# Kernel tuning notes

Measured on AMD Instinct MI355X. Metric: run time of the kernel, lower is better.

Reference implementation:

```python
import jax, jax.numpy as jnp
import numpy as np

H = 16          # num heads
DH = 64         # head size
D = H * DH      # hidden size 1024
B, S = 2, 2048


def setup_inputs() -> dict:
    key = jax.random.key(0)
    ks = jax.random.split(key, 9)
    scale = 1.0 / np.sqrt(D)
    p = {}
    p["hidden_states"] = jax.random.normal(ks[0], (B, S, D), dtype=jnp.float32)
    for i, name in enumerate(["q", "k", "v", "o"]):
        # stored so that y = x @ W + b (transpose of torch Linear weight)
        p[f"W{name}"] = jax.random.normal(ks[1 + 2 * i], (D, D), dtype=jnp.float32) * scale
        p[f"b{name}"] = jax.random.normal(ks[2 + 2 * i], (D,), dtype=jnp.float32) * 0.01
    return p


def reference(hidden_states, Wq, bq, Wk, bk, Wv, bv, Wo, bo):
    b, s, _ = hidden_states.shape
    q = hidden_states @ Wq + bq  # [B,S,D]
    k = hidden_states @ Wk + bk
    v = hidden_states @ Wv + bv
    # [B,H,S,DH]
    q = q.reshape(b, s, H, DH).transpose(0, 2, 1, 3)
    k = k.reshape(b, s, H, DH).transpose(0, 2, 1, 3)
    v = v.reshape(b, s, H, DH).transpose(0, 2, 1, 3)
    scores = jnp.einsum("bhqd,bhkd->bhqk", q, k) / np.sqrt(DH)
    causal = jnp.triu(jnp.ones((s, s), dtype=bool), k=1)  # True above diagonal -> masked
    scores = jnp.where(causal, -jnp.inf, scores)
    attn = jax.nn.softmax(scores, axis=-1)  # dropout p=0 (eval)
    ctx = jnp.einsum("bhqk,bhkd->bhqd", attn, v)
    ctx = ctx.transpose(0, 2, 1, 3).reshape(b, s, D)
    return ctx @ Wo + bo
```

## Files before the change

### kernel.cpp

```cpp
#include <hip/hip_runtime.h>


typedef _Float16 f16x8 __attribute__((ext_vector_type(8)));
typedef _Float16 f16x4 __attribute__((ext_vector_type(4)));
typedef __fp16 h16x2 __attribute__((ext_vector_type(2)));
typedef float f32x4 __attribute__((ext_vector_type(4)));
typedef float f32x16 __attribute__((ext_vector_type(16)));

#define GLD_LDS16(g, l)                                                        \
  __builtin_amdgcn_global_load_lds(                                            \
      (__attribute__((address_space(1))) const unsigned int*)(g),              \
      (__attribute__((address_space(3))) unsigned int*)(l), 16, 0, 0)

static constexpr int Sdim = 2048;
static constexpr int Ddim = 1024;
static constexpr int NH = 16;
static constexpr int DH = 64;
static constexpr int Mrows = 4096;

static constexpr float QSCALE = 0.125f * 1.44269504f;

struct PrepArgs {
  const float* X;
  _Float16* Y;
  const float *s0, *s1, *s2, *s3;
  _Float16 *d0, *d1, *d2, *d3;
};

__global__ __launch_bounds__(256) void prep(PrepArgs a) {
  __shared__ _Float16 L[64 * 72];
  const int id = blockIdx.x, t = threadIdx.x;
  if (id >= 1024) {
    size_t i = ((size_t)(id - 1024) * 256 + t) * 8;
    float4 f0 = *(const float4*)(a.X + i);
    float4 f1 = *(const float4*)(a.X + i + 4);
    alignas(16) _Float16 h[8] = {(_Float16)f0.x, (_Float16)f0.y, (_Float16)f0.z,
                                 (_Float16)f0.w, (_Float16)f1.x, (_Float16)f1.y,
                                 (_Float16)f1.z, (_Float16)f1.w};
    *(uint4*)(a.Y + i) = *(const uint4*)h;
    return;
  }
  const int z = id >> 8;
  const float* src = z == 0 ? a.s0 : z == 1 ? a.s1 : z == 2 ? a.s2 : a.s3;
  _Float16* dst = z == 0 ? a.d0 : z == 1 ? a.d1 : z == 2 ? a.d2 : a.d3;
  const int k0 = (id & 15) * 64, n0 = ((id >> 4) & 15) * 64;
#pragma unroll
  for (int i = 0; i < 4; ++i) {
    int c = i * 256 + t;
    int row = c >> 4, cc = c & 15;
    float4 f = *(const float4*)&src[(size_t)(k0 + row) * Ddim + n0 + cc * 4];
    L[(cc * 4 + 0) * 72 + row] = (_Float16)f.x;
    L[(cc * 4 + 1) * 72 + row] = (_Float16)f.y;
    L[(cc * 4 + 2) * 72 + row] = (_Float16)f.z;
    L[(cc * 4 + 3) * 72 + row] = (_Float16)f.w;
  }
  __syncthreads();
#pragma unroll
  for (int i = 0; i < 2; ++i) {
    int c = i * 256 + t;
    int n = c >> 3, cc = c & 7;
    *(uint4*)&dst[(size_t)(n0 + n) * Ddim + k0 + cc * 8] =
        *(const uint4*)&L[n * 72 + cc * 8];
  }
}

struct GemmArgs {
  const _Float16* A;
  const _Float16 *Bt0, *Bt1, *Bt2;
  const float *b0, *b1, *b2;
  void *o0, *o1, *o2;
};

template <int MODE, int BN>
__global__ __launch_bounds__(256) void gemmT(GemmArgs g) {
  constexpr int K = 1024;
  constexpr int BK = 64;
  constexpr int WN = BN / 2;
  constexpr int NI = WN / 32;
  constexpr int BCH = BN * 8;
  __shared__ _Float16 As[128 * BK];
  __shared__ _Float16 Bs[BN * BK];
  const int z = blockIdx.z;
  const _Float16* A = g.A;
  const _Float16* Bt = z == 0 ? g.Bt0 : z == 1 ? g.Bt1 : g.Bt2;
  const float* bias = z == 0 ? g.b0 : z == 1 ? g.b1 : g.b2;
  void* out = z == 0 ? g.o0 : z == 1 ? g.o1 : g.o2;
  const int m0 = blockIdx.x * 128, n0 = blockIdx.y * BN;
  const int t = threadIdx.x, lane = t & 63, wv = t >> 6;
  const int wm = wv >> 1, wn = wv & 1;
  const int n31 = lane & 31, h5 = lane >> 5, h8 = h5 * 8;

  const _Float16* ga[4];
  const _Float16* gb[4];
  char* lA[4];
  char* lB[4];
#pragma unroll
  for (int i = 0; i < 4; ++i) {
    const int c = i * 256 + t, row = c >> 3;
    ga[i] = A + (size_t)(m0 + row) * K + (((c & 7) ^ (row & 7)) * 8);
    lA[i] = (char*)As + (i * 256 + wv * 64) * 16;
  }
#pragma unroll
  for (int i = 0; i < BCH / 256; ++i) {
    const int c = i * 256 + t, row = c >> 3;
    gb[i] = Bt + (size_t)(n0 + row) * K + (((c & 7) ^ (row & 7)) * 8);
    lB[i] = (char*)Bs + (i * 256 + wv * 64) * 16;
  }
  const int rsw = (n31 & 7) << 3;

  f32x16 acc[2][NI] = {};
  for (int kt = 0; kt < K; kt += BK) {
#pragma unroll
    for (int i = 0; i < 4; ++i) GLD_LDS16(ga[i] + kt, lA[i]);
#pragma unroll
    for (int i = 0; i < BCH / 256; ++i) GLD_LDS16(gb[i] + kt, lB[i]);
    __syncthreads();
#pragma unroll
    for (int ks = 0; ks < 4; ++ks) {
      const int kc = (ks * 16 + h8) ^ rsw;
      f16x8 a0 = *(const f16x8*)&As[(wm * 64 + n31) * BK + kc];
      f16x8 a1 = *(const f16x8*)&As[(wm * 64 + 32 + n31) * BK + kc];
#pragma unroll
      for (int ni = 0; ni < NI; ++ni) {
        f16x8 bf = *(const f16x8*)&Bs[(wn * WN + ni * 32 + n31) * BK + kc];
        acc[0][ni] =
            __builtin_amdgcn_mfma_f32_32x32x16_f16(a0, bf, acc[0][ni], 0, 0, 0);
        acc[1][ni] =
            __builtin_amdgcn_mfma_f32_32x32x16_f16(a1, bf, acc[1][ni], 0, 0, 0);
      }
    }
    __syncthreads();
  }

  const float scale = (MODE == 0 && z == 0) ? QSCALE : 1.0f;
  float bv[NI];
#pragma unroll
  for (int ni = 0; ni < NI; ++ni) bv[ni] = bias[n0 + wn * WN + ni * 32 + n31];
#pragma unroll
  for (int mi = 0; mi < 2; ++mi) {
#pragma unroll
    for (int ni = 0; ni < NI; ++ni) {
      const int n = n0 + wn * WN + ni * 32 + n31;
      if (MODE == 0 && z == 2) {
        const int b = (m0 >> 11), h = n >> 6, dh = n & 63;
#pragma unroll
        for (int hi = 0; hi < 4; ++hi) {
          alignas(8) _Float16 h4[4];
#pragma unroll
          for (int j = 0; j < 4; ++j)
            h4[j] = (_Float16)(acc[mi][ni][hi * 4 + j] + bv[ni]);
          const int m = m0 + wm * 64 + mi * 32 + 8 * hi + 4 * h5;
          const int s = m & 2047;
          *(uint2*)&(
              (_Float16*)out)[((size_t)(b * NH + h) * DH + dh) * Sdim + s] =
              *(const uint2*)h4;
        }
      } else {
#pragma unroll
        for (int rr = 0; rr < 16; ++rr) {
          const int m =
              m0 + wm * 64 + mi * 32 + (rr & 3) + 8 * (rr >> 2) + 4 * h5;
          const float v = (acc[mi][ni][rr] + bv[ni]) * scale;
          if (MODE == 0) {
            const int b = m >> 11, s = m & 2047, h = n >> 6, dh = n & 63;
            ((_Float16*)out)[(((size_t)(b * NH + h) * Sdim + s) << 6) + dh] =
                (_Float16)v;
          } else {
            ((float*)out)[(size_t)m * Ddim + n] = v;
          }
        }
      }
    }
  }
}

__global__ __launch_bounds__(256) void attn(const _Float16* __restrict__ Q,
                                            const _Float16* __restrict__ Kk,
                                            const _Float16* __restrict__ Vt,
                                            _Float16* __restrict__ ctx) {
  __shared__ _Float16 Ks[2][64 * 64], Vs[2][64 * 64];
  const int id = blockIdx.x, xcd = id & 7, slot = id >> 3;
  const int qt = 31 - (slot >> 2);
  const int bh = ((slot & 3) << 3) | xcd;
  const int q0 = qt * 64;
  const int t = threadIdx.x, lane = t & 63, wv = t >> 6;
  const int qh = wv & 1, kvh = wv >> 1;
  const int n31 = lane & 31, h5 = lane >> 5, h8 = h5 * 8;
  const int b = bh >> 4, h = bh & 15;
  const _Float16* Kg = Kk + (size_t)bh * Sdim * DH;
  const _Float16* Vg = Vt + (size_t)bh * DH * Sdim;

  const int qg = q0 + qh * 32 + n31;
  const _Float16* Qrow = Q + ((size_t)bh * Sdim + qg) * DH;
  f16x8 aq[4];
#pragma unroll
  for (int ks = 0; ks < 4; ++ks) aq[ks] = *(const f16x8*)(Qrow + ks * 16 + h8);

  const int ntiles = qt + 1;
  const int sr = t >> 3, sr2 = sr + 32, sc = (t & 7) * 8;
  const int kr = (sr & 51) | ((sr & 4) << 1) | ((sr & 8) >> 1);
  const int kr2 = (sr2 & 51) | ((sr2 & 4) << 1) | ((sr2 & 8) >> 1);
  const int kc = sc ^ ((kr & 7) << 3), kc2 = sc ^ ((kr2 & 7) << 3);
  const int vc = sc ^ ((sr & 7) << 3), vc2 = sc ^ ((sr2 & 7) << 3);

  f32x16 oacc0 = {}, oacc1 = {};
  float l_i = 0.f;
  const h16x2 one2 = {(__fp16)1.0f, (__fp16)1.0f};

  uint4 ka = *(const uint4*)&Kg[(size_t)sr * DH + sc];
  uint4 kb = *(const uint4*)&Kg[(size_t)sr2 * DH + sc];
  uint4 va = *(const uint4*)&Vg[(size_t)sr * Sdim + sc];
  uint4 vb = *(const uint4*)&Vg[(size_t)sr2 * Sdim + sc];
  *(uint4*)&Ks[0][kr * 64 + kc] = ka;
  *(uint4*)&Ks[0][kr2 * 64 + kc2] = kb;
  *(uint4*)&Vs[0][sr * 64 + vc] = va;
  *(uint4*)&Vs[0][sr2 * 64 + vc2] = vb;

  const int prow = kvh * 32 + n31;
  const int pb = prow * 64, psw = (prow & 7) << 3;
  const int vsw = (n31 & 7) << 3;

  for (int it = 0; it < ntiles; ++it) {
    const int cur = it & 1;
    if (it + 1 < ntiles) {
      const int kvn = (it + 1) * 64;
      ka = *(const uint4*)&Kg[(size_t)(kvn + sr) * DH + sc];
      kb = *(const uint4*)&Kg[(size_t)(kvn + sr2) * DH + sc];
      va = *(const uint4*)&Vg[(size_t)sr * Sdim + kvn + sc];
      vb = *(const uint4*)&Vg[(size_t)sr2 * Sdim + kvn + sc];
    }
    __syncthreads();

    f32x16 sacc = {};
    __builtin_amdgcn_s_setprio(1);
#pragma unroll
    for (int ks = 0; ks < 4; ++ks) {
      f16x8 ak = *(const f16x8*)&Ks[cur][pb + ((ks * 16 + h8) ^ psw)];
      sacc = __builtin_amdgcn_mfma_f32_32x32x16_f16(ak, aq[ks], sacc, 0, 0, 0);
    }
    __builtin_amdgcn_s_setprio(0);

    const int kvb = it * 64;
    if (it == ntiles - 1) {
#pragma unroll
      for (int i = 0; i < 16; ++i) {
        const int kvgl = kvb + kvh * 32 + (i & 7) + h8 + 16 * (i >> 3);
        if (kvgl > qg) sacc[i] = -1e30f;
      }
    }
    union U { f16x8 v8; h16x2 v2[4]; } u0, u1;
#pragma unroll
    for (int i = 0; i < 4; ++i) {
      const float p0 = __builtin_amdgcn_exp2f(sacc[2 * i]);
      const float p1 = __builtin_amdgcn_exp2f(sacc[2 * i + 1]);
      u0.v2[i] = __builtin_amdgcn_cvt_pkrtz(p0, p1);
      l_i = __builtin_amdgcn_fdot2(u0.v2[i], one2, l_i, false);
    }
#pragma unroll
    for (int i = 0; i < 4; ++i) {
      const float p0 = __builtin_amdgcn_exp2f(sacc[8 + 2 * i]);
      const float p1 = __builtin_amdgcn_exp2f(sacc[9 + 2 * i]);
      u1.v2[i] = __builtin_amdgcn_cvt_pkrtz(p0, p1);
      l_i = __builtin_amdgcn_fdot2(u1.v2[i], one2, l_i, false);
    }

    __builtin_amdgcn_s_setprio(1);
#pragma unroll
    for (int ks = 0; ks < 2; ++ks) {
      const f16x8 ap = ks ? u1.v8 : u0.v8;
      const int col = kvh * 32 + ks * 16 + h8;
      f16x8 bv0 = *(const f16x8*)&Vs[cur][n31 * 64 + (col ^ vsw)];
      f16x8 bv1 = *(const f16x8*)&Vs[cur][(32 + n31) * 64 + (col ^ vsw)];
      oacc0 = __builtin_amdgcn_mfma_f32_32x32x16_f16(ap, bv0, oacc0, 0, 0, 0);
      oacc1 = __builtin_amdgcn_mfma_f32_32x32x16_f16(ap, bv1, oacc1, 0, 0, 0);
    }
    __builtin_amdgcn_s_setprio(0);

    if (it + 1 < ntiles) {
      const int nxt = cur ^ 1;
      *(uint4*)&Ks[nxt][kr * 64 + kc] = ka;
      *(uint4*)&Ks[nxt][kr2 * 64 + kc2] = kb;
      *(uint4*)&Vs[nxt][sr * 64 + vc] = va;
      *(uint4*)&Vs[nxt][sr2 * 64 + vc2] = vb;
    }
  }

  l_i += __shfl_xor(l_i, 32, 64);
  __syncthreads();
  float* obuf = (float*)&Ks[0][0] + qh * (64 * 32);
  float* lbuf = (float*)&Vs[0][0] + qh * 64;
  union V16 { f32x16 v; f32x4 q[4]; };
  if (kvh == 1) {
    V16 a, c;
    a.v = oacc0;
    c.v = oacc1;
#pragma unroll
    for (int k = 0; k < 4; ++k) {
      *(f32x4*)&obuf[lane * 32 + ((k ^ (lane & 7)) << 2)] = a.q[k];
      *(f32x4*)&obuf[lane * 32 + (((k + 4) ^ (lane & 7)) << 2)] = c.q[k];
    }
    lbuf[lane] = l_i;
  }
  __syncthreads();
  if (kvh == 0) {
    V16 a, c;
#pragma unroll
    for (int k = 0; k < 4; ++k) {
      a.q[k] = *(const f32x4*)&obuf[lane * 32 + ((k ^ (lane & 7)) << 2)];
      c.q[k] = *(const f32x4*)&obuf[lane * 32 + (((k + 4) ^ (lane & 7)) << 2)];
    }
    oacc0 += a.v;
    oacc1 += c.v;
    l_i += lbuf[lane];
#pragma unroll
    for (int rr = 0; rr < 16; ++rr) {
      const int qrow = (rr & 3) + 8 * (rr >> 2) + 4 * h5;
      const float rl = 1.0f / __shfl(l_i, qrow, 64);
      const int s = q0 + qh * 32 + qrow;
      const size_t base = ((size_t)b * Sdim + s) * Ddim + h * DH;
      ctx[base + n31] = (_Float16)(oacc0[rr] * rl);
      ctx[base + 32 + n31] = (_Float16)(oacc1[rr] * rl);
    }
  }
}

extern "C" void kernel_launch(void* const* d_in, const int* in_sizes, int n_in,
                              void* d_out, int out_size, void* d_ws,
                              size_t ws_size, hipStream_t stream) {
  const float* hid = (const float*)d_in[0];
  const float* Wq = (const float*)d_in[1];
  const float* bq = (const float*)d_in[2];
  const float* Wk = (const float*)d_in[3];
  const float* bk = (const float*)d_in[4];
  const float* Wv = (const float*)d_in[5];
  const float* bv = (const float*)d_in[6];
  const float* Wo = (const float*)d_in[7];
  const float* bo = (const float*)d_in[8];

  char* ws = (char*)d_ws;
  _Float16* Xh = (_Float16*)(ws);
  _Float16* Wqt = (_Float16*)(ws + (8ull << 20));
  _Float16* Wkt = (_Float16*)(ws + (10ull << 20));
  _Float16* Wvt = (_Float16*)(ws + (12ull << 20));
  _Float16* Wot = (_Float16*)(ws + (14ull << 20));
  _Float16* Qb = (_Float16*)(ws + (16ull << 20));
  _Float16* Kb = (_Float16*)(ws + (24ull << 20));
  _Float16* Vtb = (_Float16*)(ws + (32ull << 20));
  _Float16* ctx = Xh;

  PrepArgs pa{hid, Xh, Wq, Wk, Wv, Wo, Wqt, Wkt, Wvt, Wot};
  prep<<<dim3(3072), 256, 0, stream>>>(pa);

  GemmArgs g1{Xh, Wqt, Wkt, Wvt, bq, bk, bv, Qb, Kb, Vtb};
  gemmT<0, 128><<<dim3(Mrows / 128, Ddim / 128, 3), 256, 0, stream>>>(g1);

  attn<<<dim3(1024), 256, 0, stream>>>(Qb, Kb, Vtb, ctx);

  GemmArgs g2{ctx, Wot, Wot, Wot, bo, bo, bo, d_out, d_out, d_out};
  gemmT<1, 64><<<dim3(Mrows / 128, Ddim / 64, 1), 256, 0, stream>>>(g2);
}
```

Baseline: 171.2 us.

## Fuse prep, QKV GEMM, attention and output GEMM into one persistent megakernel

Replaces four separate kernel launches with one 1024-block persistent kernel. The phases are separated by software grid barriers built on an atomic counter stored in the output buffer, which is zeroed by a memset. The aim is to remove launch gaps and per-kernel tail effects between stages. In exchange, all 1024 blocks must be co-resident (4 blocks per CU under launch bounds), which caps register use and may cause spills in the attention phase. The barrier counter also shares memory with the final output, which the output GEMM overwrites while other blocks may still be polling it.

```diff
diff --git a/kernel.cpp b/kernel.cpp
--- a/kernel.cpp
+++ b/kernel.cpp
@@ -20,29 +20,48 @@
 
 static constexpr float QSCALE = 0.125f * 1.44269504f;
 
-struct PrepArgs {
+struct MegaArgs {
   const float* X;
-  _Float16* Y;
-  const float *s0, *s1, *s2, *s3;
-  _Float16 *d0, *d1, *d2, *d3;
+  const float* W[4];
+  const float* bqkv[3];
+  const float* bo;
+  float* out;
+  _Float16* Xh;
+  _Float16* Wt[4];
+  _Float16* QKV[3];
 };
 
-__global__ __launch_bounds__(256) void prep(PrepArgs a) {
-  __shared__ _Float16 L[64 * 72];
-  const int id = blockIdx.x, t = threadIdx.x;
-  if (id >= 1024) {
-    size_t i = ((size_t)(id - 1024) * 256 + t) * 8;
+__device__ __forceinline__ void gridbar(unsigned* cnt, unsigned target) {
+  __syncthreads();
+  if (threadIdx.x == 0) {
+    __hip_atomic_fetch_add(cnt, 1u, __ATOMIC_RELEASE,
+                           __HIP_MEMORY_SCOPE_AGENT);
+    unsigned guard = 0;
+    while (__hip_atomic_load(cnt, __ATOMIC_ACQUIRE,
+                             __HIP_MEMORY_SCOPE_AGENT) < target) {
+      __builtin_amdgcn_s_sleep(8);
+      if (++guard > (1u << 24)) break;
+    }
+  }
+  __syncthreads();
+}
+
+__device__ __forceinline__ void phase_prep(const MegaArgs& a, int id, int t,
+                                           char* smem) {
+  _Float16* L = (_Float16*)smem;
+#pragma unroll
+  for (int u = 0; u < 2; ++u) {
+    size_t i = ((size_t)(id * 2 + u) * 256 + t) * 8;
     float4 f0 = *(const float4*)(a.X + i);
     float4 f1 = *(const float4*)(a.X + i + 4);
     alignas(16) _Float16 h[8] = {(_Float16)f0.x, (_Float16)f0.y, (_Float16)f0.z,
                                  (_Float16)f0.w, (_Float16)f1.x, (_Float16)f1.y,
                                  (_Float16)f1.z, (_Float16)f1.w};
-    *(uint4*)(a.Y + i) = *(const uint4*)h;
-    return;
+    *(uint4*)(a.Xh + i) = *(const uint4*)h;
   }
   const int z = id >> 8;
-  const float* src = z == 0 ? a.s0 : z == 1 ? a.s1 : z == 2 ? a.s2 : a.s3;
-  _Float16* dst = z == 0 ? a.d0 : z == 1 ? a.d1 : z == 2 ? a.d2 : a.d3;
+  const float* src = a.W[z];
+  _Float16* dst = a.Wt[z];
   const int k0 = (id & 15) * 64, n0 = ((id >> 4) & 15) * 64;
 #pragma unroll
   for (int i = 0; i < 4; ++i) {
@@ -64,29 +83,20 @@
   }
 }
 
-struct GemmArgs {
-  const _Float16* A;
-  const _Float16 *Bt0, *Bt1, *Bt2;
-  const float *b0, *b1, *b2;
-  void *o0, *o1, *o2;
-};
-
 template <int MODE, int BN>
-__global__ __launch_bounds__(256) void gemmT(GemmArgs g) {
+__device__ __forceinline__ void phase_gemm(const _Float16* A,
+                                           const _Float16* Bt,
+                                           const float* bias, void* out,
+                                           int m0, int n0, int z, int t,
+                                           char* smem) {
   constexpr int K = 1024;
   constexpr int BK = 64;
   constexpr int WN = BN / 2;
   constexpr int NI = WN / 32;
   constexpr int BCH = BN * 8;
-  __shared__ _Float16 As[128 * BK];
-  __shared__ _Float16 Bs[BN * BK];
-  const int z = blockIdx.z;
-  const _Float16* A = g.A;
-  const _Float16* Bt = z == 0 ? g.Bt0 : z == 1 ? g.Bt1 : g.Bt2;
-  const float* bias = z == 0 ? g.b0 : z == 1 ? g.b1 : g.b2;
-  void* out = z == 0 ? g.o0 : z == 1 ? g.o1 : g.o2;
-  const int m0 = blockIdx.x * 128, n0 = blockIdx.y * BN;
-  const int t = threadIdx.x, lane = t & 63, wv = t >> 6;
+  _Float16* As = (_Float16*)smem;
+  _Float16* Bs = (_Float16*)(smem + 128 * BK * 2);
+  const int lane = t & 63, wv = t >> 6;
   const int wm = wv >> 1, wn = wv & 1;
   const int n31 = lane & 31, h5 = lane >> 5, h8 = h5 * 8;
 
@@ -174,21 +184,22 @@
   }
 }
 
-__global__ __launch_bounds__(256) void attn(const _Float16* __restrict__ Q,
-                                            const _Float16* __restrict__ Kk,
-                                            const _Float16* __restrict__ Vt,
-                                            _Float16* __restrict__ ctx) {
-  __shared__ _Float16 Ks[2][64 * 64], Vs[2][64 * 64];
-  const int id = blockIdx.x, xcd = id & 7, slot = id >> 3;
+__device__ __forceinline__ void phase_attn(const MegaArgs& a, int id, int t,
+                                           char* smem) {
+  _Float16(*Ks)[4096] = (_Float16(*)[4096])smem;
+  _Float16(*Vs)[4096] = (_Float16(*)[4096])(smem + 16384);
+  const int xcd = id & 7, slot = id >> 3;
   const int qt = 31 - (slot >> 2);
   const int bh = ((slot & 3) << 3) | xcd;
   const int q0 = qt * 64;
-  const int t = threadIdx.x, lane = t & 63, wv = t >> 6;
+  const int lane = t & 63, wv = t >> 6;
   const int qh = wv & 1, kvh = wv >> 1;
   const int n31 = lane & 31, h5 = lane >> 5, h8 = h5 * 8;
   const int b = bh >> 4, h = bh & 15;
-  const _Float16* Kg = Kk + (size_t)bh * Sdim * DH;
-  const _Float16* Vg = Vt + (size_t)bh * DH * Sdim;
+  const _Float16* Kg = a.QKV[1] + (size_t)bh * Sdim * DH;
+  const _Float16* Vg = a.QKV[2] + (size_t)bh * DH * Sdim;
+  const _Float16* Q = a.QKV[0];
+  _Float16* ctx = a.Xh;
 
   const int qg = q0 + qh * 32 + n31;
   const _Float16* Qrow = Q + ((size_t)bh * Sdim + qg) * DH;
@@ -287,30 +298,30 @@
 
   l_i += __shfl_xor(l_i, 32, 64);
   __syncthreads();
-  float* obuf = (float*)&Ks[0][0] + qh * (64 * 32);
-  float* lbuf = (float*)&Vs[0][0] + qh * 64;
+  float* obuf = (float*)smem + qh * (64 * 32);
+  float* lbuf = (float*)(smem + 16384) + qh * 64;
   union V16 { f32x16 v; f32x4 q[4]; };
   if (kvh == 1) {
-    V16 a, c;
-    a.v = oacc0;
-    c.v = oacc1;
+    V16 av, cv;
+    av.v = oacc0;
+    cv.v = oacc1;
 #pragma unroll
     for (int k = 0; k < 4; ++k) {
-      *(f32x4*)&obuf[lane * 32 + ((k ^ (lane & 7)) << 2)] = a.q[k];
-      *(f32x4*)&obuf[lane * 32 + (((k + 4) ^ (lane & 7)) << 2)] = c.q[k];
+      *(f32x4*)&obuf[lane * 32 + ((k ^ (lane & 7)) << 2)] = av.q[k];
+      *(f32x4*)&obuf[lane * 32 + (((k + 4) ^ (lane & 7)) << 2)] = cv.q[k];
     }
     lbuf[lane] = l_i;
   }
   __syncthreads();
   if (kvh == 0) {
-    V16 a, c;
+    V16 av, cv;
 #pragma unroll
     for (int k = 0; k < 4; ++k) {
-      a.q[k] = *(const f32x4*)&obuf[lane * 32 + ((k ^ (lane & 7)) << 2)];
-      c.q[k] = *(const f32x4*)&obuf[lane * 32 + (((k + 4) ^ (lane & 7)) << 2)];
-    }
-    oacc0 += a.v;
-    oacc1 += c.v;
+      av.q[k] = *(const f32x4*)&obuf[lane * 32 + ((k ^ (lane & 7)) << 2)];
+      cv.q[k] = *(const f32x4*)&obuf[lane * 32 + (((k + 4) ^ (lane & 7)) << 2)];
+    }
+    oacc0 += av.v;
+    oacc1 += cv.v;
     l_i += lbuf[lane];
 #pragma unroll
     for (int rr = 0; rr < 16; ++rr) {
@@ -324,38 +335,54 @@
   }
 }
 
+__global__ __launch_bounds__(256, 4) void mega(MegaArgs a) {
+  __shared__ alignas(16) char smem[32768];
+  unsigned* cnt = (unsigned*)a.out;
+  const int id = blockIdx.x, t = threadIdx.x;
+
+  phase_prep(a, id, t, smem);
+  gridbar(cnt, 1024);
+
+  if (id < 768) {
+    const int z = id >> 8, r = id & 255;
+    phase_gemm<0, 128>(a.Xh, a.Wt[z], a.bqkv[z], a.QKV[z], (r >> 3) * 128,
+                       (r & 7) * 128, z, t, smem);
+  }
+  gridbar(cnt, 2048);
+
+  phase_attn(a, id, t, smem);
+  gridbar(cnt, 3072);
+
+  if (id < 512) {
+    phase_gemm<1, 64>(a.Xh , a.Wt[3], a.bo, a.out, (id >> 4) * 128,
+                      (id & 15) * 64, 0, t, smem);
+  }
+}
+
 extern "C" void kernel_launch(void* const* d_in, const int* in_sizes, int n_in,
                               void* d_out, int out_size, void* d_ws,
                               size_t ws_size, hipStream_t stream) {
-  const float* hid = (const float*)d_in[0];
-  const float* Wq = (const float*)d_in[1];
-  const float* bq = (const float*)d_in[2];
-  const float* Wk = (const float*)d_in[3];
-  const float* bk = (const float*)d_in[4];
-  const float* Wv = (const float*)d_in[5];
-  const float* bv = (const float*)d_in[6];
-  const float* Wo = (const float*)d_in[7];
-  const float* bo = (const float*)d_in[8];
-
   char* ws = (char*)d_ws;
-  _Float16* Xh = (_Float16*)(ws);
-  _Float16* Wqt = (_Float16*)(ws + (8ull << 20));
-  _Float16* Wkt = (_Float16*)(ws + (10ull << 20));
-  _Float16* Wvt = (_Float16*)(ws + (12ull << 20));
-  _Float16* Wot = (_Float16*)(ws + (14ull << 20));
-  _Float16* Qb = (_Float16*)(ws + (16ull << 20));
-  _Float16* Kb = (_Float16*)(ws + (24ull << 20));
-  _Float16* Vtb = (_Float16*)(ws + (32ull << 20));
-  _Float16* ctx = Xh;
-
-  PrepArgs pa{hid, Xh, Wq, Wk, Wv, Wo, Wqt, Wkt, Wvt, Wot};
-  prep<<<dim3(3072), 256, 0, stream>>>(pa);
-
-  GemmArgs g1{Xh, Wqt, Wkt, Wvt, bq, bk, bv, Qb, Kb, Vtb};
-  gemmT<0, 128><<<dim3(Mrows / 128, Ddim / 128, 3), 256, 0, stream>>>(g1);
-
-  attn<<<dim3(1024), 256, 0, stream>>>(Qb, Kb, Vtb, ctx);
-
-  GemmArgs g2{ctx, Wot, Wot, Wot, bo, bo, bo, d_out, d_out, d_out};
-  gemmT<1, 64><<<dim3(Mrows / 128, Ddim / 64, 1), 256, 0, stream>>>(g2);
-}
+  MegaArgs ma;
+  ma.X = (const float*)d_in[0];
+  ma.W[0] = (const float*)d_in[1];
+  ma.bqkv[0] = (const float*)d_in[2];
+  ma.W[1] = (const float*)d_in[3];
+  ma.bqkv[1] = (const float*)d_in[4];
+  ma.W[2] = (const float*)d_in[5];
+  ma.bqkv[2] = (const float*)d_in[6];
+  ma.W[3] = (const float*)d_in[7];
+  ma.bo = (const float*)d_in[8];
+  ma.out = (float*)d_out;
+  ma.Xh = (_Float16*)(ws);
+  ma.Wt[0] = (_Float16*)(ws + (8ull << 20));
+  ma.Wt[1] = (_Float16*)(ws + (10ull << 20));
+  ma.Wt[2] = (_Float16*)(ws + (12ull << 20));
+  ma.Wt[3] = (_Float16*)(ws + (14ull << 20));
+  ma.QKV[0] = (_Float16*)(ws + (16ull << 20));
+  ma.QKV[1] = (_Float16*)(ws + (24ull << 20));
+  ma.QKV[2] = (_Float16*)(ws + (32ull << 20));
+
+  hipMemsetAsync(d_out, 0, 64, stream);
+  mega<<<dim3(1024), dim3(256), 0, stream>>>(ma);
+}
```

New measurement: 663.8 us. 288% more time.
